# Kernel tuning notes

Hardware: AMD Instinct MI355X
Metric: run time of the kernel (lower is better)

## Reference

```python
import jax, jax.numpy as jnp
import numpy as np
import math

B, S, D, H, L, FF = 16, 512, 1024, 16, 4, 4096
DK = D // H
EPS = 1e-5
NEG = -1e32


def make_pe(max_len, d_model):
    pos = np.arange(max_len, dtype=np.float32)[:, None]
    div = np.exp(np.arange(0, d_model, 2, dtype=np.float32) * (-math.log(10000.0) / d_model))
    pe = np.zeros((max_len, d_model), dtype=np.float32)
    pe[:, 0::2] = np.sin(pos * div)
    pe[:, 1::2] = np.cos(pos * div)
    return jnp.asarray(pe[None])  # [1, max_len, d_model]


def setup_inputs() -> dict:
    key = jax.random.key(0)
    ks = jax.random.split(key, 32)
    sd = 0.02
    inp = {
        'q_embed_data': jax.random.normal(ks[0], (B, S, D), jnp.float32),
        'qa_embed_data': jax.random.normal(ks[1], (B, S, D), jnp.float32),
        'forget_rate': jax.random.uniform(ks[2], (B, 1, S, 1), jnp.float32),
        'pe': make_pe(S, D),
        'Wk': jax.random.normal(ks[3], (L, D, D), jnp.float32) * sd,
        'bk': jnp.zeros((L, D), jnp.float32),
        'Wv': jax.random.normal(ks[4], (L, D, D), jnp.float32) * sd,
        'bv': jnp.zeros((L, D), jnp.float32),
        'Wo': jax.random.normal(ks[5], (L, D, D), jnp.float32) * sd,
        'bo': jnp.zeros((L, D), jnp.float32),
        'W1': jax.random.normal(ks[6], (L, D, FF), jnp.float32) * sd,
        'b1': jnp.zeros((L, FF), jnp.float32),
        'W2': jax.random.normal(ks[7], (L, FF, D), jnp.float32) * sd,
        'b2': jnp.zeros((L, D), jnp.float32),
        'ln1_g': jnp.ones((L, D), jnp.float32),
        'ln1_b': jnp.zeros((L, D), jnp.float32),
        'ln2_g': jnp.ones((L, D), jnp.float32),
        'ln2_b': jnp.zeros((L, D), jnp.float32),
    }
    return inp


def layernorm(x, g, b):
    m = jnp.mean(x, -1, keepdims=True)
    v = jnp.mean((x - m) ** 2, -1, keepdims=True)
    return (x - m) * jax.lax.rsqrt(v + EPS) * g + b


def forward(q_embed_data, qa_embed_data, forget_rate, pe,
            Wk, bk, Wv, bv, Wo, bo, W1, b1, W2, b2,
            ln1_g, ln1_b, ln2_g, ln2_b):
    x = q_embed_data + pe[:, :S]
    y = qa_embed_data + pe[:, :S]
    # mask==0 path: allowed positions are strictly below diagonal (j < i)
    allowed = jnp.tril(jnp.ones((S, S), bool), k=-1)
    scale = 1.0 / math.sqrt(DK)
    for l in range(L):
        # kq_same: q also uses k_linear
        k = (x @ Wk[l] + bk[l]).reshape(B, S, H, DK).transpose(0, 2, 1, 3)
        q = k
        v = (y @ Wv[l] + bv[l]).reshape(B, S, H, DK).transpose(0, 2, 1, 3)
        scores = jnp.einsum('bhid,bhjd->bhij', q, k) * scale
        scores = scores * forget_rate  # [B,1,S,1] broadcasts over heads/cols
        scores = jnp.where(allowed, scores, NEG)
        attn = jax.nn.softmax(scores, axis=-1)
        attn = attn.at[:, :, 0, :].set(0.0)  # zero_pad of first query row
        out = jnp.einsum('bhij,bhjd->bhid', attn, v)
        out = out.transpose(0, 2, 1, 3).reshape(B, S, D) @ Wo[l] + bo[l]
        x = layernorm(x + out, ln1_g[l], ln1_b[l])
        ff = jax.nn.relu(x @ W1[l] + b1[l]) @ W2[l] + b2[l]
        x = layernorm(x + ff, ln2_g[l], ln2_b[l])
    return x


def reference(q_embed_data, qa_embed_data, forget_rate, pe,
              Wk, bk, Wv, bv, Wo, bo, W1, b1, W2, b2,
              ln1_g, ln1_b, ln2_g, ln2_b):
    return forward(q_embed_data, qa_embed_data, forget_rate, pe,
                   Wk, bk, Wv, bv, Wo, bo, W1, b1, W2, b2,
                   ln1_g, ln1_b, ln2_g, ln2_b)
```

## Files before the change

### kernel.cpp

```cpp
#include <hip/hip_runtime.h>
#include <hip/hip_bf16.h>
#include <cstdint>
#include <cstddef>

#define Bq 16
#define Sq 512
#define Dq 1024
#define Hq 16
#define Lq 4
#define FFq 4096
#define Mq (Bq * Sq)

typedef unsigned short ushort_t;
typedef __attribute__((ext_vector_type(8))) short short8;
typedef __attribute__((ext_vector_type(8))) unsigned short ushortx8;
typedef __attribute__((ext_vector_type(4))) unsigned short ushortx4;
typedef __attribute__((ext_vector_type(4))) float floatx4;
typedef __attribute__((ext_vector_type(16))) float floatx16;

__device__ __forceinline__ float bf2f(ushort_t u) {
  union { unsigned int i; float f; } x;
  x.i = ((unsigned int)u) << 16;
  return x.f;
}
__device__ __forceinline__ ushort_t f2bf(float f) {
  unsigned int u = __float_as_uint(f);
  u += 0x7fffu + ((u >> 16) & 1u);
  return (ushort_t)(u >> 16);
}

#define GLL16(gp, lp) __builtin_amdgcn_global_load_lds( \
    (__attribute__((address_space(1))) void*)(gp),      \
    (__attribute__((address_space(3))) void*)(lp), 16, 0, 0)

__global__ void probe_kernel(const ushort_t* __restrict__ pe,
                             const ushort_t* __restrict__ g1,
                             int* __restrict__ flags)
{
  if (threadIdx.x == 0 && blockIdx.x == 0) {
    flags[0] = (pe[1] == (ushort_t)0x3F80u) ? 1 : 0;
    flags[1] = (g1[0] == (ushort_t)0x3F80u) ? 1 : 0;
  }
}

struct CvtArgs {
  const void* src[10];
  ushort_t*   dst[10];
  int         n[10];
  int         fi[10];
  int         cum[11];
};
__global__ __launch_bounds__(256) void convert_all_kernel(
    CvtArgs a, const int* __restrict__ flags)
{
  const int bidx = blockIdx.x;
  int s = 0;
  while (s < 9 && bidx >= a.cum[s + 1]) ++s;
  const int i = (bidx - a.cum[s]) * 256 + threadIdx.x;
  if (i >= a.n[s]) return;
  if (flags[a.fi[s]]) a.dst[s][i] = ((const ushort_t*)a.src[s])[i];
  else                a.dst[s][i] = f2bf(((const float*)a.src[s])[i]);
}

template<int BM>
__global__ __launch_bounds__(256, 2) void gemm32_kernel(
    const ushort_t* __restrict__ A0, const ushort_t* __restrict__ BT0,
    const ushort_t* __restrict__ bias0, ushort_t* __restrict__ C0,
    const ushort_t* __restrict__ A1, const ushort_t* __restrict__ BT1,
    const ushort_t* __restrict__ bias1, ushort_t* __restrict__ C1,
    int N, int K, int relu)
{
  constexpr int FR  = BM / 64;
  constexpr int CHA = BM / 64;

  __shared__ __align__(16) ushort_t As[2][BM * 32];
  __shared__ __align__(16) ushort_t Bs[2][128 * 32];

  const ushort_t* A    = blockIdx.z ? A1 : A0;
  const ushort_t* BT   = blockIdx.z ? BT1 : BT0;
  const ushort_t* bias = blockIdx.z ? bias1 : bias0;
  ushort_t*       C    = blockIdx.z ? C1 : C0;

  const int t = threadIdx.x;
  const int l = t & 63;
  const int wid = t >> 6;
  const int l31 = l & 31;
  const int wr = wid >> 1;
  const int wc = wid & 1;

  int bx = blockIdx.x, by = blockIdx.y;
  {
    const int gx = gridDim.x, gy = gridDim.y;
    if ((gy & 7) == 0) {
      const int orig = by * gx + bx;
      const int xcd = orig & 7;
      const int local = orig >> 3;
      const int rows = gy >> 3;
      by = xcd * rows + local % rows;
      bx = local / rows;
    }
  }
  const long m0 = (long)by * BM;
  const long n0 = (long)bx * 128;
  const int nk = K >> 5;

  const int rA = t >> 2;
  const int scol = (((t & 3) ^ ((rA >> 1) & 3)) << 3);
  const ushort_t* sA = A + (m0 + rA) * (long)K + scol;
  const ushort_t* sB = BT + (n0 + rA) * (long)K + scol;
  const long rs64 = 64L * (long)K;
  const int lws = wid * 512;

#define STG(buf_, kt_) do {                                            \
    const long ko_ = (long)(kt_) << 5;                                 \
    _Pragma("unroll")                                                  \
    for (int c = 0; c < CHA; ++c)                                      \
      GLL16(sA + c * rs64 + ko_, &As[(buf_)][c * 2048 + lws]);         \
    _Pragma("unroll")                                                  \
    for (int c = 0; c < 2; ++c)                                        \
      GLL16(sB + c * rs64 + ko_, &Bs[(buf_)][c * 2048 + lws]);         \
  } while (0)

  floatx16 acc[FR][2];
#pragma unroll
  for (int i = 0; i < FR; ++i)
#pragma unroll
    for (int j = 0; j < 2; ++j)
#pragma unroll
      for (int r = 0; r < 16; ++r) acc[i][j][r] = 0.0f;

  const int xo = (l >> 1) & 3;
  const int co0 = (((l >> 5)) ^ xo) << 3;
  const int co1 = ((2 + (l >> 5)) ^ xo) << 3;
  const int arow = wr * (BM / 2) + l31;
  const int brow = wc * 64 + l31;

  STG(0, 0);
  __syncthreads();

  for (int kt = 0; kt < nk; ++kt) {
    const int buf = kt & 1;
    if (kt + 1 < nk) STG(buf ^ 1, kt + 1);

    short8 a[FR][2], b[2][2];
#pragma unroll
    for (int fr = 0; fr < FR; ++fr) {
      a[fr][0] = *(const short8*)&As[buf][(arow + fr * 32) * 32 + co0];
      a[fr][1] = *(const short8*)&As[buf][(arow + fr * 32) * 32 + co1];
    }
#pragma unroll
    for (int fc = 0; fc < 2; ++fc) {
      b[fc][0] = *(const short8*)&Bs[buf][(brow + fc * 32) * 32 + co0];
      b[fc][1] = *(const short8*)&Bs[buf][(brow + fc * 32) * 32 + co1];
    }

#pragma unroll
    for (int sl = 0; sl < 2; ++sl)
#pragma unroll
      for (int fc = 0; fc < 2; ++fc)
#pragma unroll
        for (int fr = 0; fr < FR; ++fr)
          acc[fr][fc] = __builtin_amdgcn_mfma_f32_32x32x16_bf16(
              a[fr][sl], b[fc][sl], acc[fr][fc], 0, 0, 0);

    __syncthreads();
  }
#undef STG

#pragma unroll
  for (int fc = 0; fc < 2; ++fc) {
    const long col = n0 + wc * 64 + fc * 32 + l31;
    const float bsv = bf2f(bias[col]);
#pragma unroll
    for (int fr = 0; fr < FR; ++fr) {
      const floatx16 v = acc[fr][fc];
      const long rbase = m0 + wr * (BM / 2) + fr * 32 + 4 * (l >> 5);
#pragma unroll
      for (int r = 0; r < 16; ++r) {
        const long row = rbase + (r & 3) + 8 * (r >> 2);
        float x = v[r] + bsv;
        if (relu) x = fmaxf(x, 0.0f);
        C[row * N + col] = f2bf(x);
      }
    }
  }
}

__global__ __launch_bounds__(256) void attn_kernel(
    const ushort_t* __restrict__ kq, const ushort_t* __restrict__ vt,
    const ushort_t* __restrict__ fr, ushort_t* __restrict__ ao)
{
  __shared__ __align__(16) ushort_t P[4][64 * 72];
  const int t = threadIdx.x;
  const int lane = t & 63;
  const int w4 = t >> 6;
  const int wq = blockIdx.y * 4 + w4;
  const int b = blockIdx.x >> 4;
  const int h = blockIdx.x & 15;
  const int la = lane & 15;
  const int lb = lane >> 4;
  const int i0 = wq * 64;
  const long kbase = ((long)b * Sq) * Dq + h * 64;
  const long vbase = ((long)(b * Hq + h)) * (64L * Sq);

  short8 qf[4][2];
#pragma unroll
  for (int mf = 0; mf < 4; ++mf)
#pragma unroll
    for (int tt = 0; tt < 2; ++tt)
      qf[mf][tt] = *(const short8*)&kq[kbase + (long)(i0 + mf * 16 + la) * Dq + tt * 32 + lb * 8];

  float frs[4][4];
#pragma unroll
  for (int mf = 0; mf < 4; ++mf)
#pragma unroll
    for (int r = 0; r < 4; ++r)
      frs[mf][r] = 0.125f * bf2f(fr[b * Sq + i0 + mf * 16 + lb * 4 + r]);

  const floatx4 z4 = {0.f, 0.f, 0.f, 0.f};
  floatx4 o[4][4];
  float mrun[4][4], lrun[4][4];
#pragma unroll
  for (int mf = 0; mf < 4; ++mf)
#pragma unroll
    for (int x = 0; x < 4; ++x) {
      o[mf][x] = z4;
      mrun[mf][x] = -1e30f;
      lrun[mf][x] = 0.0f;
    }

  for (int jt = 0; jt <= wq; ++jt) {
    const int j0 = jt * 64;
    floatx4 s[4][4];
#pragma unroll
    for (int mf = 0; mf < 4; ++mf)
#pragma unroll
      for (int jf = 0; jf < 4; ++jf) s[mf][jf] = z4;

#pragma unroll
    for (int tt = 0; tt < 2; ++tt) {
      short8 kf[4];
#pragma unroll
      for (int jf = 0; jf < 4; ++jf)
        kf[jf] = *(const short8*)&kq[kbase + (long)(j0 + jf * 16 + la) * Dq + tt * 32 + lb * 8];
#pragma unroll
      for (int mf = 0; mf < 4; ++mf)
#pragma unroll
        for (int jf = 0; jf < 4; ++jf)
          s[mf][jf] = __builtin_amdgcn_mfma_f32_16x16x32_bf16(qf[mf][tt], kf[jf], s[mf][jf], 0, 0, 0);
    }

    const bool diag = (jt == wq);
#pragma unroll
    for (int mf = 0; mf < 4; ++mf)
#pragma unroll
      for (int jf = 0; jf < 4; ++jf)
#pragma unroll
        for (int r = 0; r < 4; ++r) {
          float x = s[mf][jf][r] * frs[mf][r];
          if (diag && (j0 + jf * 16 + la) >= (i0 + mf * 16 + lb * 4 + r)) x = -1e30f;
          s[mf][jf][r] = x;
        }

#pragma unroll
    for (int mf = 0; mf < 4; ++mf)
#pragma unroll
      for (int r = 0; r < 4; ++r) {
        float pm = fmaxf(fmaxf(s[mf][0][r], s[mf][1][r]), fmaxf(s[mf][2][r], s[mf][3][r]));
        pm = fmaxf(pm, __shfl_xor(pm, 1));
        pm = fmaxf(pm, __shfl_xor(pm, 2));
        pm = fmaxf(pm, __shfl_xor(pm, 4));
        pm = fmaxf(pm, __shfl_xor(pm, 8));
        const float mo = mrun[mf][r];
        const float mn = fmaxf(mo, pm);
        const float sc = __expf(mo - mn);
        mrun[mf][r] = mn;
        float rs = 0.0f;
#pragma unroll
        for (int jf = 0; jf < 4; ++jf) {
          const float p = __expf(s[mf][jf][r] - mn);
          s[mf][jf][r] = p;
          rs += p;
        }
        rs += __shfl_xor(rs, 1);
        rs += __shfl_xor(rs, 2);
        rs += __shfl_xor(rs, 4);
        rs += __shfl_xor(rs, 8);
        lrun[mf][r] = lrun[mf][r] * sc + rs;
#pragma unroll
        for (int df = 0; df < 4; ++df) o[mf][df][r] *= sc;
      }

#pragma unroll
    for (int mf = 0; mf < 4; ++mf)
#pragma unroll
      for (int jf = 0; jf < 4; ++jf)
#pragma unroll
        for (int r = 0; r < 4; ++r)
          P[w4][(mf * 16 + lb * 4 + r) * 72 + jf * 16 + la] = f2bf(s[mf][jf][r]);

#pragma unroll
    for (int tt = 0; tt < 2; ++tt) {
      short8 pf[4], vf[4];
#pragma unroll
      for (int mf = 0; mf < 4; ++mf)
        pf[mf] = *(const short8*)&P[w4][(mf * 16 + la) * 72 + tt * 32 + lb * 8];
#pragma unroll
      for (int df = 0; df < 4; ++df)
        vf[df] = *(const short8*)&vt[vbase + (long)(df * 16 + la) * Sq + j0 + tt * 32 + lb * 8];
#pragma unroll
      for (int mf = 0; mf < 4; ++mf)
#pragma unroll
        for (int df = 0; df < 4; ++df)
          o[mf][df] = __builtin_amdgcn_mfma_f32_16x16x32_bf16(pf[mf], vf[df], o[mf][df], 0, 0, 0);
    }
  }

#pragma unroll
  for (int mf = 0; mf < 4; ++mf)
#pragma unroll
    for (int df = 0; df < 4; ++df)
#pragma unroll
      for (int r = 0; r < 4; ++r) {
        const int ii = i0 + mf * 16 + lb * 4 + r;
        const float vv = (ii == 0) ? 0.0f : o[mf][df][r] / lrun[mf][r];
        ao[((long)b * Sq + ii) * Dq + h * 64 + df * 16 + la] = f2bf(vv);
      }
}

__global__ __launch_bounds__(256) void ln_kernel(
    float* __restrict__ xf, const ushort_t* __restrict__ add,
    const ushort_t* __restrict__ g, const ushort_t* __restrict__ bb,
    ushort_t* __restrict__ outb, float* __restrict__ outf,
    const int* __restrict__ flags, int final_)
{
  __shared__ float red[2][4];
  const long row = blockIdx.x;
  const int t = threadIdx.x;
  const int c = t * 4;
  float* xr = xf + row * Dq;
  const ushort_t* ar = add + row * Dq;

  floatx4 xv = *(floatx4*)&xr[c];
  ushortx4 av = *(const ushortx4*)&ar[c];
  float v[4];
  float s1 = 0.f, s2 = 0.f;
#pragma unroll
  for (int e = 0; e < 4; ++e) {
    v[e] = xv[e] + bf2f(av[e]);
    s1 += v[e];
    s2 += v[e] * v[e];
  }
#pragma unroll
  for (int m = 1; m < 64; m <<= 1) {
    s1 += __shfl_xor(s1, m);
    s2 += __shfl_xor(s2, m);
  }
  const int lane = t & 63, w = t >> 6;
  if (lane == 0) { red[0][w] = s1; red[1][w] = s2; }
  __syncthreads();
  s1 = red[0][0] + red[0][1] + red[0][2] + red[0][3];
  s2 = red[1][0] + red[1][1] + red[1][2] + red[1][3];
  const float mean = s1 * (1.0f / Dq);
  const float var = fmaxf(s2 * (1.0f / Dq) - mean * mean, 0.0f);
  const float rstd = rsqrtf(var + 1e-5f);
  ushortx4 gv = *(const ushortx4*)&g[c];
  ushortx4 bv = *(const ushortx4*)&bb[c];
  ushortx4 ob;
  floatx4 xo;
#pragma unroll
  for (int e = 0; e < 4; ++e) {
    const float y = (v[e] - mean) * rstd * bf2f(gv[e]) + bf2f(bv[e]);
    xo[e] = y;
    ob[e] = f2bf(y);
  }
  *(floatx4*)&xr[c] = xo;
  if (final_ && !flags[0]) {
    *(floatx4*)&outf[row * Dq + c] = xo;
  } else {
    *(ushortx4*)&outb[row * Dq + c] = ob;
  }
}

__global__ __launch_bounds__(256) void addpe_kernel(
    const void* __restrict__ qe, const void* __restrict__ qa,
    const void* __restrict__ pe, float* __restrict__ xf,
    ushort_t* __restrict__ xb, ushort_t* __restrict__ yb,
    const int* __restrict__ flags)
{
  const long i = ((long)blockIdx.x * 256 + threadIdx.x) * 8;
  const long sd = i & ((long)Sq * Dq - 1);
  const bool isb = flags[0] != 0;
  float q[8], a[8], p[8];
  if (isb) {
    ushortx8 q8 = *(const ushortx8*)((const ushort_t*)qe + i);
    ushortx8 a8 = *(const ushortx8*)((const ushort_t*)qa + i);
    ushortx8 p8 = *(const ushortx8*)((const ushort_t*)pe + sd);
#pragma unroll
    for (int e = 0; e < 8; ++e) { q[e] = bf2f(q8[e]); a[e] = bf2f(a8[e]); p[e] = bf2f(p8[e]); }
  } else {
    const float* qp = (const float*)qe + i;
    const float* ap = (const float*)qa + i;
    const float* pp = (const float*)pe + sd;
    floatx4 q0 = *(const floatx4*)qp, q1 = *(const floatx4*)(qp + 4);
    floatx4 a0 = *(const floatx4*)ap, a1 = *(const floatx4*)(ap + 4);
    floatx4 p0 = *(const floatx4*)pp, p1 = *(const floatx4*)(pp + 4);
#pragma unroll
    for (int e = 0; e < 4; ++e) {
      q[e] = q0[e]; q[e + 4] = q1[e];
      a[e] = a0[e]; a[e + 4] = a1[e];
      p[e] = p0[e]; p[e + 4] = p1[e];
    }
  }
  ushortx8 xo, yo;
  floatx4 f0, f1;
#pragma unroll
  for (int e = 0; e < 8; ++e) {
    const float xvv = (isb ? q[e] : bf2f(f2bf(q[e]))) + (isb ? p[e] : bf2f(f2bf(p[e])));
    const float yvv = (isb ? a[e] : bf2f(f2bf(a[e]))) + (isb ? p[e] : bf2f(f2bf(p[e])));
    if (e < 4) { f0[e] = xvv; } else { f1[e - 4] = xvv; }
    xo[e] = f2bf(xvv);
    yo[e] = f2bf(yvv);
  }
  *(floatx4*)&xf[i] = f0;
  *(floatx4*)&xf[i + 4] = f1;
  *(ushortx8*)&xb[i] = xo;
  *(ushortx8*)&yb[i] = yo;
}

__global__ __launch_bounds__(256) void transpose_kernel(
    const void* __restrict__ src, ushort_t* __restrict__ dst, int K, int N,
    const int* __restrict__ flags)
{
  __shared__ __align__(16) ushort_t tile[64][72];
  const bool isb = flags[1] != 0;
  const long base = (long)blockIdx.z * K * N;
  const int k0 = blockIdx.y * 64, n0 = blockIdx.x * 64;
  const int t = threadIdx.x;
  const int r = t >> 3;
  const int cc = (t & 7) << 3;
#pragma unroll
  for (int it = 0; it < 2; ++it) {
    const int rr = r + it * 32;
    const long gi = base + (long)(k0 + rr) * N + n0 + cc;
    if (isb) {
      *(short8*)&tile[rr][cc] = *(const short8*)((const ushort_t*)src + gi);
    } else {
      const float* sf = (const float*)src + gi;
      floatx4 v0 = *(const floatx4*)sf;
      floatx4 v1 = *(const floatx4*)(sf + 4);
#pragma unroll
      for (int e = 0; e < 4; ++e) {
        tile[rr][cc + e] = f2bf(v0[e]);
        tile[rr][cc + 4 + e] = f2bf(v1[e]);
      }
    }
  }
  __syncthreads();
#pragma unroll
  for (int it = 0; it < 2; ++it) {
    const int rr = r + it * 32;
    short8 v;
#pragma unroll
    for (int e = 0; e < 8; ++e) v[e] = (short)tile[cc + e][rr];
    *(short8*)&dst[base + (long)(n0 + rr) * K + k0 + cc] = v;
  }
}

__global__ __launch_bounds__(256) void vtrans_kernel(
    const ushort_t* __restrict__ vb, ushort_t* __restrict__ vt)
{
  __shared__ __align__(16) ushort_t tile[64][72];
  const int b = blockIdx.y >> 4, h = blockIdx.y & 15;
  const int j0 = blockIdx.x * 64;
  const int t = threadIdx.x;
  const int r = t >> 3;
  const int cc = (t & 7) << 3;
#pragma unroll
  for (int it = 0; it < 2; ++it) {
    const int rr = r + it * 32;
    *(short8*)&tile[rr][cc] = *(const short8*)&vb[((long)b * Sq + j0 + rr) * Dq + h * 64 + cc];
  }
  __syncthreads();
#pragma unroll
  for (int it = 0; it < 2; ++it) {
    const int rr = r + it * 32;
    short8 v;
#pragma unroll
    for (int e = 0; e < 8; ++e) v[e] = (short)tile[cc + e][rr];
    *(short8*)&vt[((long)(b * Hq + h) * 64 + rr) * Sq + j0 + cc] = v;
  }
}

extern "C" void kernel_launch(void* const* d_in, const int* in_sizes, int n_in,
                              void* d_out, int out_size, void* d_ws, size_t ws_size,
                              hipStream_t stream)
{
  if (n_in < 18) return;
  const void* qe  = d_in[0];
  const void* qa  = d_in[1];
  const void* fr  = d_in[2];
  const void* pe  = d_in[3];
  const void* Wk  = d_in[4];
  const void* bk  = d_in[5];
  const void* Wv  = d_in[6];
  const void* bv  = d_in[7];
  const void* Wo  = d_in[8];
  const void* bo  = d_in[9];
  const void* W1  = d_in[10];
  const void* b1  = d_in[11];
  const void* W2  = d_in[12];
  const void* b2  = d_in[13];
  const void* g1  = d_in[14];
  const void* be1 = d_in[15];
  const void* g2  = d_in[16];
  const void* be2 = d_in[17];

  char* ws = (char*)d_ws;
  const size_t SM = 243269632L;
  const size_t NEED = SM + 114752L;
  if (ws_size < NEED) return;

  float*    xf   = (float*)   (ws + 0L);
  ushort_t* xb   = (ushort_t*)(ws + 33554432L);
  ushort_t* yb   = (ushort_t*)(ws + 50331648L);
  ushort_t* tmpD = (ushort_t*)(ws + 67108864L);
  ushort_t* WkT  = (ushort_t*)(ws + 83886080L);
  ushort_t* WvT  = (ushort_t*)(ws + 92274688L);
  ushort_t* WoT  = (ushort_t*)(ws + 100663296L);
  ushort_t* W1T  = (ushort_t*)(ws + 109051904L);
  ushort_t* W2T  = (ushort_t*)(ws + 142606336L);
  ushort_t* kb   = (ushort_t*)(ws + 176160768L);
  ushort_t* vbf  = (ushort_t*)(ws + 192937984L);
  ushort_t* vtb  = (ushort_t*)(ws + 209715200L);
  ushort_t* ff1  = kb;

  int*      flags = (int*)(ws + SM);
  ushort_t* frc  = (ushort_t*)(ws + SM + 64);
  ushort_t* bkc  = (ushort_t*)(ws + SM + 16448);
  ushort_t* bvc  = (ushort_t*)(ws + SM + 24640);
  ushort_t* boc  = (ushort_t*)(ws + SM + 32832);
  ushort_t* b1c  = (ushort_t*)(ws + SM + 41024);
  ushort_t* b2c  = (ushort_t*)(ws + SM + 73792);
  ushort_t* g1c  = (ushort_t*)(ws + SM + 81984);
  ushort_t* be1c = (ushort_t*)(ws + SM + 90176);
  ushort_t* g2c  = (ushort_t*)(ws + SM + 98368);
  ushort_t* be2c = (ushort_t*)(ws + SM + 106560);

  probe_kernel<<<1, 64, 0, stream>>>((const ushort_t*)pe, (const ushort_t*)g1, flags);

  {
    CvtArgs a;
    const void* srcs[10] = {fr, bk, bv, bo, b1, b2, g1, be1, g2, be2};
    ushort_t*   dsts[10] = {frc, bkc, bvc, boc, b1c, b2c, g1c, be1c, g2c, be2c};
    const int   ns[10]   = {8192, 4096, 4096, 4096, 16384, 4096, 4096, 4096, 4096, 4096};
    int cum = 0;
    for (int s = 0; s < 10; ++s) {
      a.src[s] = srcs[s]; a.dst[s] = dsts[s]; a.n[s] = ns[s];
      a.fi[s] = (s == 0) ? 0 : 1;
      a.cum[s] = cum;
      cum += (ns[s] + 255) / 256;
    }
    a.cum[10] = cum;
    convert_all_kernel<<<cum, 256, 0, stream>>>(a, flags);
  }

  transpose_kernel<<<dim3(16, 16, 4), 256, 0, stream>>>(Wk, WkT, 1024, 1024, flags);
  transpose_kernel<<<dim3(16, 16, 4), 256, 0, stream>>>(Wv, WvT, 1024, 1024, flags);
  transpose_kernel<<<dim3(16, 16, 4), 256, 0, stream>>>(Wo, WoT, 1024, 1024, flags);
  transpose_kernel<<<dim3(64, 16, 4), 256, 0, stream>>>(W1, W1T, 1024, 4096, flags);
  transpose_kernel<<<dim3(16, 64, 4), 256, 0, stream>>>(W2, W2T, 4096, 1024, flags);

  addpe_kernel<<<4096, 256, 0, stream>>>(qe, qa, pe, xf, xb, yb, flags);

  for (int l = 0; l < 4; ++l) {
    gemm32_kernel<256><<<dim3(8, 32, 2), 256, 0, stream>>>(
        xb, WkT + (long)l * 1048576, bkc + l * 1024, kb,
        yb, WvT + (long)l * 1048576, bvc + l * 1024, vbf,
        1024, 1024, 0);
    vtrans_kernel<<<dim3(8, 256), 256, 0, stream>>>(vbf, vtb);
    attn_kernel<<<dim3(256, 2), 256, 0, stream>>>(kb, vtb, frc, vbf);
    gemm32_kernel<128><<<dim3(8, 64, 1), 256, 0, stream>>>(
        vbf, WoT + (long)l * 1048576, boc + l * 1024, tmpD,
        vbf, WoT + (long)l * 1048576, boc + l * 1024, tmpD,
        1024, 1024, 0);
    ln_kernel<<<8192, 256, 0, stream>>>(xf, tmpD, g1c + l * 1024, be1c + l * 1024, xb, nullptr, flags, 0);
    gemm32_kernel<256><<<dim3(32, 32, 1), 256, 0, stream>>>(
        xb, W1T + (long)l * 4194304, b1c + l * 4096, ff1,
        xb, W1T + (long)l * 4194304, b1c + l * 4096, ff1,
        4096, 1024, 1);
    gemm32_kernel<128><<<dim3(8, 64, 1), 256, 0, stream>>>(
        ff1, W2T + (long)l * 4194304, b2c + l * 1024, tmpD,
        ff1, W2T + (long)l * 4194304, b2c + l * 1024, tmpD,
        1024, 4096, 0);
    if (l == 3) {
      ln_kernel<<<8192, 256, 0, stream>>>(xf, tmpD, g2c + l * 1024, be2c + l * 1024,
                                          (ushort_t*)d_out, (float*)d_out, flags, 1);
    } else {
      ln_kernel<<<8192, 256, 0, stream>>>(xf, tmpD, g2c + l * 1024, be2c + l * 1024,
                                          xb, nullptr, flags, 0);
    }
  }
}
```

Before: 1.716 ms.

## Use 128x128 GEMM tiles and split-K the N=1024 GEMMs across two halves

Replaces the templated GEMM with a single 128x128-tile kernel at higher occupancy (launch bounds 4). The Wo and W2 projections now split K in two along the z dimension. The second half writes a bias-free partial into the xb buffer, and the LayerNorm kernel sums both partials. The aim is more parallelism for the N=1024 GEMMs, which previously launched only 512 blocks. The cost is extra partial-sum traffic and the reuse of xb as scratch.

Result: faster. 1.641 ms (-4.3%).

```diff
diff --git a/kernel.cpp b/kernel.cpp
--- a/kernel.cpp
+++ b/kernel.cpp
@@ -62,24 +62,21 @@
   else                a.dst[s][i] = f2bf(((const float*)a.src[s])[i]);
 }
 
-template<int BM>
-__global__ __launch_bounds__(256, 2) void gemm32_kernel(
+__global__ __launch_bounds__(256, 4) void gemm128_kernel(
     const ushort_t* __restrict__ A0, const ushort_t* __restrict__ BT0,
-    const ushort_t* __restrict__ bias0, ushort_t* __restrict__ C0,
+    const ushort_t* __restrict__ bias0, ushort_t* __restrict__ C0, int koff0,
     const ushort_t* __restrict__ A1, const ushort_t* __restrict__ BT1,
-    const ushort_t* __restrict__ bias1, ushort_t* __restrict__ C1,
-    int N, int K, int relu)
-{
-  constexpr int FR  = BM / 64;
-  constexpr int CHA = BM / 64;
-
-  __shared__ __align__(16) ushort_t As[2][BM * 32];
+    const ushort_t* __restrict__ bias1, ushort_t* __restrict__ C1, int koff1,
+    int N, int Kst, int Klen, int relu)
+{
+  __shared__ __align__(16) ushort_t As[2][128 * 32];
   __shared__ __align__(16) ushort_t Bs[2][128 * 32];
 
   const ushort_t* A    = blockIdx.z ? A1 : A0;
   const ushort_t* BT   = blockIdx.z ? BT1 : BT0;
   const ushort_t* bias = blockIdx.z ? bias1 : bias0;
   ushort_t*       C    = blockIdx.z ? C1 : C0;
+  const int       koff = blockIdx.z ? koff1 : koff0;
 
   const int t = threadIdx.x;
   const int l = t & 63;
@@ -100,30 +97,28 @@
       bx = local / rows;
     }
   }
-  const long m0 = (long)by * BM;
+  const long m0 = (long)by * 128;
   const long n0 = (long)bx * 128;
-  const int nk = K >> 5;
+  const int nk = Klen >> 5;
 
   const int rA = t >> 2;
   const int scol = (((t & 3) ^ ((rA >> 1) & 3)) << 3);
-  const ushort_t* sA = A + (m0 + rA) * (long)K + scol;
-  const ushort_t* sB = BT + (n0 + rA) * (long)K + scol;
-  const long rs64 = 64L * (long)K;
+  const ushort_t* sA = A + (m0 + rA) * (long)Kst + koff + scol;
+  const ushort_t* sB = BT + (n0 + rA) * (long)Kst + koff + scol;
+  const long rs64 = 64L * (long)Kst;
   const int lws = wid * 512;
 
 #define STG(buf_, kt_) do {                                            \
     const long ko_ = (long)(kt_) << 5;                                 \
-    _Pragma("unroll")                                                  \
-    for (int c = 0; c < CHA; ++c)                                      \
-      GLL16(sA + c * rs64 + ko_, &As[(buf_)][c * 2048 + lws]);         \
-    _Pragma("unroll")                                                  \
-    for (int c = 0; c < 2; ++c)                                        \
-      GLL16(sB + c * rs64 + ko_, &Bs[(buf_)][c * 2048 + lws]);         \
+    GLL16(sA + ko_,        &As[(buf_)][lws]);                          \
+    GLL16(sA + rs64 + ko_, &As[(buf_)][2048 + lws]);                   \
+    GLL16(sB + ko_,        &Bs[(buf_)][lws]);                          \
+    GLL16(sB + rs64 + ko_, &Bs[(buf_)][2048 + lws]);                   \
   } while (0)
 
-  floatx16 acc[FR][2];
-#pragma unroll
-  for (int i = 0; i < FR; ++i)
+  floatx16 acc[2][2];
+#pragma unroll
+  for (int i = 0; i < 2; ++i)
 #pragma unroll
     for (int j = 0; j < 2; ++j)
 #pragma unroll
@@ -132,7 +127,7 @@
   const int xo = (l >> 1) & 3;
   const int co0 = (((l >> 5)) ^ xo) << 3;
   const int co1 = ((2 + (l >> 5)) ^ xo) << 3;
-  const int arow = wr * (BM / 2) + l31;
+  const int arow = wr * 64 + l31;
   const int brow = wc * 64 + l31;
 
   STG(0, 0);
@@ -142,9 +137,9 @@
     const int buf = kt & 1;
     if (kt + 1 < nk) STG(buf ^ 1, kt + 1);
 
-    short8 a[FR][2], b[2][2];
-#pragma unroll
-    for (int fr = 0; fr < FR; ++fr) {
+    short8 a[2][2], b[2][2];
+#pragma unroll
+    for (int fr = 0; fr < 2; ++fr) {
       a[fr][0] = *(const short8*)&As[buf][(arow + fr * 32) * 32 + co0];
       a[fr][1] = *(const short8*)&As[buf][(arow + fr * 32) * 32 + co1];
     }
@@ -159,7 +154,7 @@
 #pragma unroll
       for (int fc = 0; fc < 2; ++fc)
 #pragma unroll
-        for (int fr = 0; fr < FR; ++fr)
+        for (int fr = 0; fr < 2; ++fr)
           acc[fr][fc] = __builtin_amdgcn_mfma_f32_32x32x16_bf16(
               a[fr][sl], b[fc][sl], acc[fr][fc], 0, 0, 0);
 
@@ -170,11 +165,11 @@
 #pragma unroll
   for (int fc = 0; fc < 2; ++fc) {
     const long col = n0 + wc * 64 + fc * 32 + l31;
-    const float bsv = bf2f(bias[col]);
-#pragma unroll
-    for (int fr = 0; fr < FR; ++fr) {
+    const float bsv = bias ? bf2f(bias[col]) : 0.0f;
+#pragma unroll
+    for (int fr = 0; fr < 2; ++fr) {
       const floatx16 v = acc[fr][fc];
-      const long rbase = m0 + wr * (BM / 2) + fr * 32 + 4 * (l >> 5);
+      const long rbase = m0 + wr * 64 + fr * 32 + 4 * (l >> 5);
 #pragma unroll
       for (int r = 0; r < 16; ++r) {
         const long row = rbase + (r & 3) + 8 * (r >> 2);
@@ -330,6 +325,7 @@
 
 __global__ __launch_bounds__(256) void ln_kernel(
     float* __restrict__ xf, const ushort_t* __restrict__ add,
+    const ushort_t* __restrict__ add2,
     const ushort_t* __restrict__ g, const ushort_t* __restrict__ bb,
     ushort_t* __restrict__ outb, float* __restrict__ outf,
     const int* __restrict__ flags, int final_)
@@ -343,11 +339,15 @@
 
   floatx4 xv = *(floatx4*)&xr[c];
   ushortx4 av = *(const ushortx4*)&ar[c];
+  ushortx4 a2v;
+  if (add2) a2v = *(const ushortx4*)&add2[row * Dq + c];
   float v[4];
   float s1 = 0.f, s2 = 0.f;
 #pragma unroll
   for (int e = 0; e < 4; ++e) {
-    v[e] = xv[e] + bf2f(av[e]);
+    float av_ = bf2f(av[e]);
+    if (add2) av_ += bf2f(a2v[e]);
+    v[e] = xv[e] + av_;
     s1 += v[e];
     s2 += v[e] * v[e];
   }
@@ -574,30 +574,31 @@
   addpe_kernel<<<4096, 256, 0, stream>>>(qe, qa, pe, xf, xb, yb, flags);
 
   for (int l = 0; l < 4; ++l) {
-    gemm32_kernel<256><<<dim3(8, 32, 2), 256, 0, stream>>>(
-        xb, WkT + (long)l * 1048576, bkc + l * 1024, kb,
-        yb, WvT + (long)l * 1048576, bvc + l * 1024, vbf,
-        1024, 1024, 0);
+    gemm128_kernel<<<dim3(8, 64, 2), 256, 0, stream>>>(
+        xb, WkT + (long)l * 1048576, bkc + l * 1024, kb, 0,
+        yb, WvT + (long)l * 1048576, bvc + l * 1024, vbf, 0,
+        1024, 1024, 1024, 0);
     vtrans_kernel<<<dim3(8, 256), 256, 0, stream>>>(vbf, vtb);
     attn_kernel<<<dim3(256, 2), 256, 0, stream>>>(kb, vtb, frc, vbf);
-    gemm32_kernel<128><<<dim3(8, 64, 1), 256, 0, stream>>>(
-        vbf, WoT + (long)l * 1048576, boc + l * 1024, tmpD,
-        vbf, WoT + (long)l * 1048576, boc + l * 1024, tmpD,
-        1024, 1024, 0);
-    ln_kernel<<<8192, 256, 0, stream>>>(xf, tmpD, g1c + l * 1024, be1c + l * 1024, xb, nullptr, flags, 0);
-    gemm32_kernel<256><<<dim3(32, 32, 1), 256, 0, stream>>>(
-        xb, W1T + (long)l * 4194304, b1c + l * 4096, ff1,
-        xb, W1T + (long)l * 4194304, b1c + l * 4096, ff1,
-        4096, 1024, 1);
-    gemm32_kernel<128><<<dim3(8, 64, 1), 256, 0, stream>>>(
-        ff1, W2T + (long)l * 4194304, b2c + l * 1024, tmpD,
-        ff1, W2T + (long)l * 4194304, b2c + l * 1024, tmpD,
-        1024, 4096, 0);
+    gemm128_kernel<<<dim3(8, 64, 2), 256, 0, stream>>>(
+        vbf, WoT + (long)l * 1048576, boc + l * 1024, tmpD, 0,
+        vbf, WoT + (long)l * 1048576, nullptr,        xb,   512,
+        1024, 1024, 512, 0);
+    ln_kernel<<<8192, 256, 0, stream>>>(xf, tmpD, xb, g1c + l * 1024, be1c + l * 1024,
+                                        xb, nullptr, flags, 0);
+    gemm128_kernel<<<dim3(32, 64, 1), 256, 0, stream>>>(
+        xb, W1T + (long)l * 4194304, b1c + l * 4096, ff1, 0,
+        xb, W1T + (long)l * 4194304, b1c + l * 4096, ff1, 0,
+        4096, 1024, 1024, 1);
+    gemm128_kernel<<<dim3(8, 64, 2), 256, 0, stream>>>(
+        ff1, W2T + (long)l * 4194304, b2c + l * 1024, tmpD, 0,
+        ff1, W2T + (long)l * 4194304, nullptr,        xb,   2048,
+        1024, 4096, 2048, 0);
     if (l == 3) {
-      ln_kernel<<<8192, 256, 0, stream>>>(xf, tmpD, g2c + l * 1024, be2c + l * 1024,
+      ln_kernel<<<8192, 256, 0, stream>>>(xf, tmpD, xb, g2c + l * 1024, be2c + l * 1024,
                                           (ushort_t*)d_out, (float*)d_out, flags, 1);
     } else {
-      ln_kernel<<<8192, 256, 0, stream>>>(xf, tmpD, g2c + l * 1024, be2c + l * 1024,
+      ln_kernel<<<8192, 256, 0, stream>>>(xf, tmpD, xb, g2c + l * 1024, be2c + l * 1024,
                                           xb, nullptr, flags, 0);
     }
   }
```
